# Kernel optimization log

Measured on AMD Instinct MI355X. Metric: run time of the kernel, lower is better.

## Reference

```python
import jax, jax.numpy as jnp
import numpy as np


def _positional_embedding(C, M, dtype):
    # pe[pos, 0::2] = sin(pos*div), pe[pos, 1::2] = cos(pos*div)
    pos = jnp.arange(M, dtype=jnp.float32)[:, None]                      # [M,1]
    div = jnp.exp(jnp.arange(0, C, 2, dtype=jnp.float32) * (-np.log(10000.0) / C))  # [C/2]
    ang = pos * div                                                      # [M,C/2]
    pe = jnp.stack([jnp.sin(ang), jnp.cos(ang)], axis=-1).reshape(M, C)  # interleave
    return pe.T.astype(dtype)                                            # [C,M]


def setup_inputs() -> dict:
    key = jax.random.key(0)
    k1, k2, k3 = jax.random.split(key, 3)
    B, C, M, K = 64, 512, 1024, 5
    h_in = jax.random.normal(k1, (B, C, 1, M), dtype=jnp.float32)
    conv_w = jax.random.normal(k2, (C, K), dtype=jnp.float32) * 0.1
    conv_b = jax.random.normal(k3, (C,), dtype=jnp.float32) * 0.1
    return {"h_in": h_in, "conv_w": conv_w, "conv_b": conv_b}


def reference(h_in, conv_w, conv_b):
    B, C, _, M = h_in.shape
    K = conv_w.shape[1]
    p = (K - 1) // 2
    dt = h_in.dtype

    hb = h_in                                              # pre-PE copy
    pe = _positional_embedding(C, M, dt)                   # [C,M]
    x = h_in + pe[None, :, None, :]                        # [B,C,1,M]

    # adaptive avg pool to 1 over (H,W)
    y = jnp.mean(x, axis=(2, 3))                           # [B,C]
    # unfold along channel axis with padding p, window K
    y_pad = jnp.pad(y, ((0, 0), (p, p)))                   # [B,C+2p]
    idx = jnp.arange(C)[:, None] + jnp.arange(K)[None, :]  # [C,K]
    y_unf = y_pad[:, idx]                                  # [B,C,K]
    # grouped conv1d -> per-channel dot over window, then sigmoid gate
    gate = jax.nn.sigmoid(jnp.einsum('bck,ck->bc', y_unf, conv_w) + conv_b)  # [B,C]

    h = x * gate[:, :, None, None]                         # dropout = identity (eval)

    hs = h[:, :, 0, :]                                     # [B,C,M]
    hbs = hb[:, :, 0, :]                                   # [B,C,M]
    I_hat = (jnp.eye(M, dtype=dt) / M) - (1.0 / (M * M))   # [M,M] centering matrix

    t1 = jnp.einsum('bcm,mn->bcn', hs, I_hat)
    t2 = jnp.einsum('bcm,mn->bcn', hbs, I_hat)
    cov = (jnp.einsum('bcn,bdn->bcd', t1, hs)
           + jnp.einsum('bcn,bdn->bcd', t2, hbs)
           + jnp.eye(C, dtype=dt) * 1e-8)                  # [B,C,C]
    return cov
```

## Files before the change

kernel.cpp:

```cpp
#include <hip/hip_runtime.h>
#include <math.h>

#define B_N 64
#define C_N 512
#define M_N 1024
#define K_W 2048

typedef __attribute__((ext_vector_type(8))) short bf16x8;
typedef __attribute__((ext_vector_type(4))) float f32x4;

__device__ __forceinline__ unsigned short f2b(float f) {
  unsigned int x = __builtin_bit_cast(unsigned int, f);
  unsigned int lsb = (x >> 16) & 1u;
  x += 0x7fffu + lsb;
  return (unsigned short)(x >> 16);
}

typedef __attribute__((address_space(1))) const unsigned int gas_uint;
typedef __attribute__((address_space(3))) unsigned int las_uint;
__device__ __forceinline__ void async_ld(const void* g, const void* l) {
  __builtin_amdgcn_global_load_lds((gas_uint*)(uintptr_t)g,
                                   (las_uint*)(unsigned int)(uintptr_t)l, 16, 0, 0);
}

__global__ void k_pe(float* __restrict__ pe, float* __restrict__ pesum) {
  int c = blockIdx.x, m = threadIdx.x;
  float freq = expf((float)(c & ~1) * (-9.210340371976184f / 512.0f));
  float ang = (float)m * freq;
  float v = (c & 1) ? cosf(ang) : sinf(ang);
  pe[c * M_N + m] = v;
  float s = v;
  for (int off = 32; off; off >>= 1) s += __shfl_down(s, off);
  __shared__ float ws[16];
  if ((m & 63) == 0) ws[m >> 6] = s;
  __syncthreads();
  if (m < 16) {
    float t = ws[m];
    for (int off = 8; off; off >>= 1) t += __shfl_down(t, off);
    if (m == 0) pesum[c] = t;
  }
}

__global__ void k_rs(const float* __restrict__ src, float* __restrict__ rb) {
  __shared__ float ws[4];
  int t = threadIdx.x;
  size_t e = ((size_t)blockIdx.x * 256 + t) * 8;
  const float4* s4 = (const float4*)(src + e);
  float4 v0 = s4[0], v1 = s4[1];
  float s = v0.x + v0.y + v0.z + v0.w + v1.x + v1.y + v1.z + v1.w;
  for (int off = 32; off; off >>= 1) s += __shfl_down(s, off);
  if ((t & 63) == 0) ws[t >> 6] = s;
  __syncthreads();
  if (t == 0) rb[blockIdx.x * 2] = ws[0] + ws[1];
  if (t == 128) rb[blockIdx.x * 2 + 1] = ws[2] + ws[3];
}

__global__ void k_gate(const float* __restrict__ wp, const float* __restrict__ bp,
                       const float* __restrict__ rb0, const float* __restrict__ pesum,
                       float* __restrict__ u, float* __restrict__ rbF,
                       float* __restrict__ gateF) {
  int idx = blockIdx.x * 256 + threadIdx.x;
  int b = idx >> 9, c = idx & (C_N - 1);
  float rbv = rb0[idx];
  float rx = rbv + pesum[c];
  float acc = 0.f;
  for (int k = 0; k < 5; ++k) {
    int cc = c + k - 2;
    if (cc < 0 || cc >= C_N) continue;
    float y = (rb0[b * C_N + cc] + pesum[cc]) * (1.0f / 1024.0f);
    acc += y * wp[c * 5 + k];
  }
  float g = 1.0f / (1.0f + expf(-(acc + bp[c])));
  gateF[idx] = g;
  u[idx] = g * rx;
  rbF[idx] = rbv;
}

__global__ void k_x(const float* __restrict__ src, unsigned short* __restrict__ Wd,
                    const float* __restrict__ pe, const float* __restrict__ gateF) {
  int row = blockIdx.x;
  int c = row & (C_N - 1), t = threadIdx.x;
  const float* rp = src + (size_t)row * M_N;
  float4 h4 = ((const float4*)rp)[t];
  float4 p4 = ((const float4*)(pe + (size_t)c * M_N))[t];
  float g = gateF[row];
  union { uint2 v; unsigned short us[4]; } H, X;
  H.us[0] = f2b(h4.x); H.us[1] = f2b(h4.y); H.us[2] = f2b(h4.z); H.us[3] = f2b(h4.w);
  X.us[0] = f2b(g * (h4.x + p4.x)); X.us[1] = f2b(g * (h4.y + p4.y));
  X.us[2] = f2b(g * (h4.z + p4.z)); X.us[3] = f2b(g * (h4.w + p4.w));
  __syncthreads();
  unsigned short* wr = Wd + (size_t)row * K_W;
  ((uint2*)wr)[t] = H.v;
  ((uint2*)(wr + M_N))[t] = X.v;
}

__device__ __forceinline__ void cov_stage(unsigned short (*tl)[128 * 32],
                                          const unsigned short* srcp, int wsel) {
  for (int g = 0; g < 8; g++)
    async_ld(srcp + (size_t)g * (16 * K_W), &tl[wsel][g * 512]);
}

template <int VM, bool STG, int CUR>
__device__ __forceinline__ void cov_step(
    unsigned short (*tiles)[2][128 * 32], int it, const unsigned short* srcp,
    int wsel, int wc, int fr, int fcol, f32x4 (&acc)[8][4]) {
  asm volatile("s_waitcnt vmcnt(%0)" ::"n"(VM) : "memory");
  __builtin_amdgcn_sched_barrier(0);
  __builtin_amdgcn_s_barrier();
  __builtin_amdgcn_sched_barrier(0);
  bf16x8 bf[4], af[8];
  for (int j = 0; j < 4; j++)
    bf[j] = *(const bf16x8*)&tiles[CUR][1][(wc + j * 16 + fr) * 32 + fcol];
  for (int i = 0; i < 8; i++)
    af[i] = *(const bf16x8*)&tiles[CUR][0][(i * 16 + fr) * 32 + fcol];
  if (STG)
    cov_stage(tiles[(CUR + 2) % 3], srcp + (size_t)(it + 2) * 32, wsel);
  asm volatile("s_waitcnt lgkmcnt(0)" ::: "memory");
  __builtin_amdgcn_sched_barrier(0);
  __builtin_amdgcn_s_setprio(1);
  for (int i = 0; i < 8; i++)
    for (int j = 0; j < 4; j++)
      acc[i][j] = __builtin_amdgcn_mfma_f32_16x16x32_bf16(af[i], bf[j], acc[i][j], 0, 0, 0);
  __builtin_amdgcn_s_setprio(0);
}

__global__ __launch_bounds__(128, 2)
void k_cov(const unsigned short* __restrict__ W, const float* __restrict__ aux,
           float* __restrict__ out, int b0, int bpx) {
  __shared__ unsigned short tiles[3][2][128 * 32];
  int t = threadIdx.x, lane = t & 63, w = t >> 6;
  int bid = blockIdx.x;
  int xcd = bid & 7, i5 = bid >> 3;
  int b = b0 + xcd * bpx + i5 / 10;
  int s = i5 % 10;
  int ti = (s >= 1) + (s >= 3) + (s >= 6);
  int tj = s - ti * (ti + 1) / 2;
  int cblk = ti * 128, dblk = tj * 128;

  int rowbase = w ? dblk : cblk;
  int wsel = w;
  int gcol = (lane & 3) ^ ((lane >> 3) & 3);
  const unsigned short* srcp = W + (size_t)b * (C_N * K_W)
      + (size_t)(rowbase + (lane >> 2)) * K_W + gcol * 8;

  int wc = w * 64;
  int fr = lane & 15, kc = lane >> 4;
  int fcol = (kc ^ ((fr >> 1) & 3)) * 8;

  f32x4 acc[8][4];
  const f32x4 z = {0.f, 0.f, 0.f, 0.f};
  for (int i = 0; i < 8; i++) for (int j = 0; j < 4; j++) acc[i][j] = z;

  cov_stage(tiles[0], srcp, wsel);
  cov_stage(tiles[1], srcp + 32, wsel);

  for (int it = 0; it < 60; it += 3) {
    cov_step<8, true, 0>(tiles, it + 0, srcp, wsel, wc, fr, fcol, acc);
    cov_step<8, true, 1>(tiles, it + 1, srcp, wsel, wc, fr, fcol, acc);
    cov_step<8, true, 2>(tiles, it + 2, srcp, wsel, wc, fr, fcol, acc);
  }
  cov_step<8, true, 0>(tiles, 60, srcp, wsel, wc, fr, fcol, acc);
  cov_step<8, true, 1>(tiles, 61, srcp, wsel, wc, fr, fcol, acc);
  cov_step<8, false, 2>(tiles, 62, srcp, wsel, wc, fr, fcol, acc);
  cov_step<0, false, 0>(tiles, 63, srcp, wsel, wc, fr, fcol, acc);

  const float invM = 1.0f / 1024.0f, invM2 = invM * invM;
  const float* ub = aux + (size_t)b * C_N;
  const float* rbb = aux + (size_t)B_N * C_N + (size_t)b * C_N;
  for (int i = 0; i < 8; i++)
    for (int r = 0; r < 4; r++) {
      int c = cblk + i * 16 + kc * 4 + r;
      float uc = ub[c], rbc = rbb[c];
      for (int j = 0; j < 4; j++) {
        int d = dblk + wc + j * 16 + fr;
        float v = acc[i][j][r] * invM - (uc * ub[d] + rbc * rbb[d]) * invM2;
        if (c == d) v += 1e-8f;
        out[((size_t)b * C_N + c) * C_N + d] = v;
      }
    }

  if (ti != tj) {
    float* tb = (float*)tiles;
    for (int hp = 0; hp < 2; ++hp) {
      __syncthreads();
      for (int i = hp * 4; i < hp * 4 + 4; i++)
        for (int j = 0; j < 4; j++)
          for (int r = 0; r < 4; r++) {
            int ch = i * 16 + kc * 4 + r - hp * 64;
            int dl = wc + j * 16 + fr;
            tb[ch * 128 + (dl ^ (ch & 31))] = acc[i][j][r];
          }
      __syncthreads();
      for (int p = 0; p < 16; ++p) {
        int dl = p * 8 + (t >> 4);
        int cl = (t & 15) * 4;
        int dg = dblk + dl;
        float ud = ub[dg], rbd = rbb[dg];
        float4 o;
        float* op = (float*)&o;
        for (int q = 0; q < 4; ++q) {
          int cg = cblk + hp * 64 + cl + q;
          float raw = tb[(cl + q) * 128 + (dl ^ ((cl + q) & 31))];
          op[q] = raw * invM - (ub[cg] * ud + rbb[cg] * rbd) * invM2;
        }
        *(float4*)&out[((size_t)b * C_N + dg) * C_N + (cblk + hp * 64 + cl)] = o;
      }
    }
  }
}

extern "C" void kernel_launch(void* const* d_in, const int* in_sizes, int n_in,
                              void* d_out, int out_size, void* d_ws, size_t ws_size,
                              hipStream_t stream) {
  const float* h32 = (const float*)d_in[0];
  const float* conv_w = (const float*)d_in[1];
  const float* conv_b = (const float*)d_in[2];
  char* OUT = (char*)d_out;
  char* HIN = (char*)d_in[0];

  char* SCR = OUT + (48ull << 20);
  float* rb0   = (float*)SCR;
  float* pesum = (float*)(SCR + (128 << 10));
  float* gateF = (float*)(SCR + (192 << 10));
  float* peF   = (float*)(OUT + (49ull << 20));

  bool ws_ok = (d_ws != nullptr) && (ws_size >= (size_t)(256 << 10));
  float* uX = ws_ok ? (float*)d_ws : (float*)(SCR + (512 << 10));

  k_pe<<<C_N, 1024, 0, stream>>>(peF, pesum);
  k_rs<<<16384, 256, 0, stream>>>(h32, rb0);
  k_gate<<<(B_N * C_N) / 256, 256, 0, stream>>>(conv_w, conv_b, rb0, pesum,
                                                uX, uX + B_N * C_N, gateF);
  k_x<<<B_N * C_N, 256, 0, stream>>>(h32, (unsigned short*)HIN, peF, gateF);

  if (ws_ok) {
    k_cov<<<640, 128, 0, stream>>>((const unsigned short*)HIN, uX,
                                   (float*)d_out, 0, 8);
  } else {
    k_cov<<<320, 128, 0, stream>>>((const unsigned short*)HIN, uX,
                                   (float*)d_out, 0, 4);
    hipMemcpyAsync(HIN, uX, 256 << 10, hipMemcpyDeviceToDevice, stream);
    k_cov<<<320, 128, 0, stream>>>((const unsigned short*)HIN, (const float*)HIN,
                                   (float*)d_out, 32, 4);
  }
}
```

Baseline: 306.6 us.

## Replace 128x128 two-wave cov GEMM with 256x256 eight-wave tile kernel

Rewrites the batched covariance GEMM kernel so each block uses 8 waves on a 256x256 output tile (3 tiles per batch with symmetry) with BK=64 double-buffered LDS and a quad-phased MFMA schedule that interleaves async global->LDS loads. The larger tile is meant to improve operand reuse and reduce global traffic per FLOP versus 128x128 tiles with 2 waves. In exchange it launches only 192 blocks, which is under one wave of work on a 256-CU device, and uses a larger LDS footprint. The transposed-store epilogue is also reworked to use a padded stride.

```diff
diff --git a/kernel.cpp b/kernel.cpp
--- a/kernel.cpp
+++ b/kernel.cpp
@@ -5,6 +5,8 @@
 #define C_N 512
 #define M_N 1024
 #define K_W 2048
+#define BK 64
+#define NT 32
 
 typedef __attribute__((ext_vector_type(8))) short bf16x8;
 typedef __attribute__((ext_vector_type(4))) float f32x4;
@@ -94,85 +96,139 @@
   ((uint2*)(wr + M_N))[t] = X.v;
 }
 
-__device__ __forceinline__ void cov_stage(unsigned short (*tl)[128 * 32],
-                                          const unsigned short* srcp, int wsel) {
-  for (int g = 0; g < 8; g++)
-    async_ld(srcp + (size_t)g * (16 * K_W), &tl[wsel][g * 512]);
-}
-
-template <int VM, bool STG, int CUR>
-__device__ __forceinline__ void cov_step(
-    unsigned short (*tiles)[2][128 * 32], int it, const unsigned short* srcp,
-    int wsel, int wc, int fr, int fcol, f32x4 (&acc)[8][4]) {
-  asm volatile("s_waitcnt vmcnt(%0)" ::"n"(VM) : "memory");
-  __builtin_amdgcn_sched_barrier(0);
+__device__ __forceinline__ bf16x8 MF(bf16x8 a, bf16x8 b, f32x4& c) {
+  c = __builtin_amdgcn_mfma_f32_16x16x32_bf16(a, b, c, 0, 0, 0);
+  return a;
+}
+
+template <int QUAD, bool RDB, bool STG, int VMN>
+__device__ __forceinline__ void phase(
+    const short* lA, const short* lB, const unsigned short* ssrc, short* sdst,
+    int wm, int wn, int fr, int chA0, int chA1,
+    bf16x8 (&bfr)[4][2], f32x4 (&acc)[8][4]) {
+  bf16x8 af[2][2];
+  int r0 = (wm * 128 + QUAD * 32 + fr) * BK;
+  af[0][0] = *(const bf16x8*)&lA[r0 + chA0 * 8];
+  af[0][1] = *(const bf16x8*)&lA[r0 + chA1 * 8];
+  af[1][0] = *(const bf16x8*)&lA[r0 + 16 * BK + chA0 * 8];
+  af[1][1] = *(const bf16x8*)&lA[r0 + 16 * BK + chA1 * 8];
+  if constexpr (RDB) {
+#pragma unroll
+    for (int j = 0; j < 4; j++) {
+      int rb = (wn * 64 + j * 16 + fr) * BK;
+      bfr[j][0] = *(const bf16x8*)&lB[rb + chA0 * 8];
+      bfr[j][1] = *(const bf16x8*)&lB[rb + chA1 * 8];
+    }
+  }
+  if constexpr (STG) {
+    async_ld(ssrc, sdst);
+    async_ld(ssrc + 8 * K_W, sdst + 8 * BK);
+  }
   __builtin_amdgcn_s_barrier();
   __builtin_amdgcn_sched_barrier(0);
-  bf16x8 bf[4], af[8];
-  for (int j = 0; j < 4; j++)
-    bf[j] = *(const bf16x8*)&tiles[CUR][1][(wc + j * 16 + fr) * 32 + fcol];
-  for (int i = 0; i < 8; i++)
-    af[i] = *(const bf16x8*)&tiles[CUR][0][(i * 16 + fr) * 32 + fcol];
-  if (STG)
-    cov_stage(tiles[(CUR + 2) % 3], srcp + (size_t)(it + 2) * 32, wsel);
   asm volatile("s_waitcnt lgkmcnt(0)" ::: "memory");
   __builtin_amdgcn_sched_barrier(0);
   __builtin_amdgcn_s_setprio(1);
-  for (int i = 0; i < 8; i++)
-    for (int j = 0; j < 4; j++)
-      acc[i][j] = __builtin_amdgcn_mfma_f32_16x16x32_bf16(af[i], bf[j], acc[i][j], 0, 0, 0);
+#pragma unroll
+  for (int i2 = 0; i2 < 2; i2++)
+#pragma unroll
+    for (int j = 0; j < 4; j++) {
+      acc[QUAD * 2 + i2][j] = __builtin_amdgcn_mfma_f32_16x16x32_bf16(
+          af[i2][0], bfr[j][0], acc[QUAD * 2 + i2][j], 0, 0, 0);
+      acc[QUAD * 2 + i2][j] = __builtin_amdgcn_mfma_f32_16x16x32_bf16(
+          af[i2][1], bfr[j][1], acc[QUAD * 2 + i2][j], 0, 0, 0);
+    }
   __builtin_amdgcn_s_setprio(0);
-}
-
-__global__ __launch_bounds__(128, 2)
-void k_cov(const unsigned short* __restrict__ W, const float* __restrict__ aux,
-           float* __restrict__ out, int b0, int bpx) {
-  __shared__ unsigned short tiles[3][2][128 * 32];
+  if constexpr (VMN >= 0) {
+    asm volatile("s_waitcnt vmcnt(%0)" ::"n"(VMN) : "memory");
+    __builtin_amdgcn_sched_barrier(0);
+  }
+  __builtin_amdgcn_s_barrier();
+  __builtin_amdgcn_sched_barrier(0);
+}
+
+__global__ __launch_bounds__(512, 2)
+void k_cov8(const unsigned short* __restrict__ W, const float* __restrict__ aux,
+            float* __restrict__ out, int b0, int bpx) {
+  __shared__ short lds[2][2][256 * BK];
   int t = threadIdx.x, lane = t & 63, w = t >> 6;
+  int wm = w >> 2, wn = w & 3;
+  int fr = lane & 15, kc = lane >> 4;
   int bid = blockIdx.x;
-  int xcd = bid & 7, i5 = bid >> 3;
-  int b = b0 + xcd * bpx + i5 / 10;
-  int s = i5 % 10;
-  int ti = (s >= 1) + (s >= 3) + (s >= 6);
-  int tj = s - ti * (ti + 1) / 2;
-  int cblk = ti * 128, dblk = tj * 128;
-
-  int rowbase = w ? dblk : cblk;
-  int wsel = w;
-  int gcol = (lane & 3) ^ ((lane >> 3) & 3);
-  const unsigned short* srcp = W + (size_t)b * (C_N * K_W)
-      + (size_t)(rowbase + (lane >> 2)) * K_W + gcol * 8;
-
-  int wc = w * 64;
-  int fr = lane & 15, kc = lane >> 4;
-  int fcol = (kc ^ ((fr >> 1) & 3)) * 8;
+  int xcd = bid & 7, i3 = bid >> 3;
+  int b = b0 + xcd * bpx + i3 / 3;
+  int s = i3 % 3;
+  int ti = (s + 1) >> 1, tj = s >> 1;
+  int cblk = ti * 256, dblk = tj * 256;
+
+  int lr = lane >> 3, lc = lane & 7;
+  const unsigned short* baseW = W + (size_t)b * (C_N * K_W);
+  const unsigned short* srcA = baseW + (size_t)(cblk + lr) * K_W + (lc ^ lr) * 8;
+  const unsigned short* srcB = baseW + (size_t)(dblk + lr) * K_W + (lc ^ lr) * 8;
+  int chA0 = kc ^ (fr & 7);
+  int chA1 = (4 + kc) ^ (fr & 7);
+  int rw0 = w * 16;
 
   f32x4 acc[8][4];
   const f32x4 z = {0.f, 0.f, 0.f, 0.f};
-  for (int i = 0; i < 8; i++) for (int j = 0; j < 4; j++) acc[i][j] = z;
-
-  cov_stage(tiles[0], srcp, wsel);
-  cov_stage(tiles[1], srcp + 32, wsel);
-
-  for (int it = 0; it < 60; it += 3) {
-    cov_step<8, true, 0>(tiles, it + 0, srcp, wsel, wc, fr, fcol, acc);
-    cov_step<8, true, 1>(tiles, it + 1, srcp, wsel, wc, fr, fcol, acc);
-    cov_step<8, true, 2>(tiles, it + 2, srcp, wsel, wc, fr, fcol, acc);
-  }
-  cov_step<8, true, 0>(tiles, 60, srcp, wsel, wc, fr, fcol, acc);
-  cov_step<8, true, 1>(tiles, 61, srcp, wsel, wc, fr, fcol, acc);
-  cov_step<8, false, 2>(tiles, 62, srcp, wsel, wc, fr, fcol, acc);
-  cov_step<0, false, 0>(tiles, 63, srcp, wsel, wc, fr, fcol, acc);
+#pragma unroll
+  for (int i = 0; i < 8; i++)
+#pragma unroll
+    for (int j = 0; j < 4; j++) acc[i][j] = z;
+  bf16x8 bfr[4][2];
+
+#define SRC_A(h, kt) (srcA + (size_t)((h)*128 + rw0) * K_W + (kt)*BK)
+#define SRC_B(h, kt) (srcB + (size_t)((h)*128 + rw0) * K_W + (kt)*BK)
+#define DST(buf, op, h) (&lds[buf][op][((h)*128 + rw0) * BK])
+#define STG2(buf, op, h, srcp)            \
+  {                                       \
+    const unsigned short* _s = (srcp);    \
+    short* _d = DST(buf, op, h);          \
+    async_ld(_s, _d);                     \
+    async_ld(_s + 8 * K_W, _d + 8 * BK);  \
+  }
+
+  STG2(0, 0, 0, SRC_A(0, 0)); STG2(0, 0, 1, SRC_A(1, 0));
+  STG2(0, 1, 0, SRC_B(0, 0)); STG2(0, 1, 1, SRC_B(1, 0));
+  STG2(1, 1, 0, SRC_B(0, 1)); STG2(1, 1, 1, SRC_B(1, 1));
+  asm volatile("s_waitcnt vmcnt(4)" ::: "memory");
+  __builtin_amdgcn_sched_barrier(0);
+  __builtin_amdgcn_s_barrier();
+  __builtin_amdgcn_sched_barrier(0);
+
+  for (int n = 0; n < 15; ++n) {
+    int kt0 = 2 * n, kt1 = 2 * n + 1;
+    phase<0, true,  true, -1>(lds[0][0], lds[0][1], SRC_A(0, kt1), DST(1, 0, 0), wm, wn, fr, chA0, chA1, bfr, acc);
+    phase<1, false, true, -1>(lds[0][0], lds[0][1], SRC_A(1, kt1), DST(1, 0, 1), wm, wn, fr, chA0, chA1, bfr, acc);
+    phase<2, false, true, -1>(lds[0][0], lds[0][1], SRC_B(0, kt0 + 2), DST(0, 1, 0), wm, wn, fr, chA0, chA1, bfr, acc);
+    phase<3, false, true,  4>(lds[0][0], lds[0][1], SRC_B(1, kt0 + 2), DST(0, 1, 1), wm, wn, fr, chA0, chA1, bfr, acc);
+    phase<0, true,  true, -1>(lds[1][0], lds[1][1], SRC_A(0, kt0 + 2), DST(0, 0, 0), wm, wn, fr, chA0, chA1, bfr, acc);
+    phase<1, false, true, -1>(lds[1][0], lds[1][1], SRC_A(1, kt0 + 2), DST(0, 0, 1), wm, wn, fr, chA0, chA1, bfr, acc);
+    phase<2, false, true, -1>(lds[1][0], lds[1][1], SRC_B(0, kt1 + 2), DST(1, 1, 0), wm, wn, fr, chA0, chA1, bfr, acc);
+    phase<3, false, true,  4>(lds[1][0], lds[1][1], SRC_B(1, kt1 + 2), DST(1, 1, 1), wm, wn, fr, chA0, chA1, bfr, acc);
+  }
+  phase<0, true,  true, -1>(lds[0][0], lds[0][1], SRC_A(0, 31), DST(1, 0, 0), wm, wn, fr, chA0, chA1, bfr, acc);
+  phase<1, false, true, -1>(lds[0][0], lds[0][1], SRC_A(1, 31), DST(1, 0, 1), wm, wn, fr, chA0, chA1, bfr, acc);
+  phase<2, false, false, -1>(lds[0][0], lds[0][1], nullptr, nullptr, wm, wn, fr, chA0, chA1, bfr, acc);
+  phase<3, false, false,  0>(lds[0][0], lds[0][1], nullptr, nullptr, wm, wn, fr, chA0, chA1, bfr, acc);
+  phase<0, true,  false, -1>(lds[1][0], lds[1][1], nullptr, nullptr, wm, wn, fr, chA0, chA1, bfr, acc);
+  phase<1, false, false, -1>(lds[1][0], lds[1][1], nullptr, nullptr, wm, wn, fr, chA0, chA1, bfr, acc);
+  phase<2, false, false, -1>(lds[1][0], lds[1][1], nullptr, nullptr, wm, wn, fr, chA0, chA1, bfr, acc);
+  phase<3, false, false, -1>(lds[1][0], lds[1][1], nullptr, nullptr, wm, wn, fr, chA0, chA1, bfr, acc);
 
   const float invM = 1.0f / 1024.0f, invM2 = invM * invM;
   const float* ub = aux + (size_t)b * C_N;
   const float* rbb = aux + (size_t)B_N * C_N + (size_t)b * C_N;
+
+#pragma unroll
   for (int i = 0; i < 8; i++)
+#pragma unroll
     for (int r = 0; r < 4; r++) {
-      int c = cblk + i * 16 + kc * 4 + r;
+      int c = cblk + wm * 128 + i * 16 + kc * 4 + r;
       float uc = ub[c], rbc = rbb[c];
+#pragma unroll
       for (int j = 0; j < 4; j++) {
-        int d = dblk + wc + j * 16 + fr;
+        int d = dblk + wn * 64 + j * 16 + fr;
         float v = acc[i][j][r] * invM - (uc * ub[d] + rbc * rbb[d]) * invM2;
         if (c == d) v += 1e-8f;
         out[((size_t)b * C_N + c) * C_N + d] = v;
@@ -180,33 +236,42 @@
     }
 
   if (ti != tj) {
-    float* tb = (float*)tiles;
-    for (int hp = 0; hp < 2; ++hp) {
+    float* tb = (float*)lds;
+    for (int ch = 0; ch < 4; ++ch) {
       __syncthreads();
-      for (int i = hp * 4; i < hp * 4 + 4; i++)
-        for (int j = 0; j < 4; j++)
-          for (int r = 0; r < 4; r++) {
-            int ch = i * 16 + kc * 4 + r - hp * 64;
-            int dl = wc + j * 16 + fr;
-            tb[ch * 128 + (dl ^ (ch & 31))] = acc[i][j][r];
-          }
+      if (wm == (ch >> 1)) {
+        int i0 = (ch & 1) * 4;
+#pragma unroll
+        for (int i2 = 0; i2 < 4; i2++)
+#pragma unroll
+          for (int j = 0; j < 4; j++)
+#pragma unroll
+            for (int r = 0; r < 4; r++)
+              tb[(i2 * 16 + kc * 4 + r) * 257 + wn * 64 + j * 16 + fr] =
+                  acc[i0 + i2][j][r];
+      }
       __syncthreads();
-      for (int p = 0; p < 16; ++p) {
-        int dl = p * 8 + (t >> 4);
+      for (int p = 0; p < 8; ++p) {
+        int dl = p * 32 + (t >> 4);
         int cl = (t & 15) * 4;
         int dg = dblk + dl;
         float ud = ub[dg], rbd = rbb[dg];
         float4 o;
         float* op = (float*)&o;
+#pragma unroll
         for (int q = 0; q < 4; ++q) {
-          int cg = cblk + hp * 64 + cl + q;
-          float raw = tb[(cl + q) * 128 + (dl ^ ((cl + q) & 31))];
+          int cg = cblk + ch * 64 + cl + q;
+          float raw = tb[(cl + q) * 257 + dl];
           op[q] = raw * invM - (ub[cg] * ud + rbb[cg] * rbd) * invM2;
         }
-        *(float4*)&out[((size_t)b * C_N + dg) * C_N + (cblk + hp * 64 + cl)] = o;
+        *(float4*)&out[((size_t)b * C_N + dg) * C_N + (cblk + ch * 64 + cl)] = o;
       }
     }
   }
+#undef SRC_A
+#undef SRC_B
+#undef DST
+#undef STG2
 }
 
 extern "C" void kernel_launch(void* const* d_in, const int* in_sizes, int n_in,
@@ -234,13 +299,13 @@
   k_x<<<B_N * C_N, 256, 0, stream>>>(h32, (unsigned short*)HIN, peF, gateF);
 
   if (ws_ok) {
-    k_cov<<<640, 128, 0, stream>>>((const unsigned short*)HIN, uX,
-                                   (float*)d_out, 0, 8);
+    k_cov8<<<192, 512, 0, stream>>>((const unsigned short*)HIN, uX,
+                                    (float*)d_out, 0, 8);
   } else {
-    k_cov<<<320, 128, 0, stream>>>((const unsigned short*)HIN, uX,
+    k_cov8<<<96, 512, 0, stream>>>((const unsigned short*)HIN, uX,
                                    (float*)d_out, 0, 4);
     hipMemcpyAsync(HIN, uX, 256 << 10, hipMemcpyDeviceToDevice, stream);
-    k_cov<<<320, 128, 0, stream>>>((const unsigned short*)HIN, (const float*)HIN,
+    k_cov8<<<96, 512, 0, stream>>>((const unsigned short*)HIN, (const float*)HIN,
                                    (float*)d_out, 32, 4);
   }
 }
```

Measured after the change: 307.3 us. About the same (+0.2%).
